# Optimization experiments

Measured on AMD Instinct MI355X. Metric: run time of the kernel, lower is better.

Reference implementation:

```python
import jax, jax.numpy as jnp
import numpy as np

B, L, D = 2, 2048, 2048
H, KV, HD = 16, 8, 128
EPS = 1e-5
ROPE_BASE = 10000.0
SCALING_ALPHA = 1.0
SCALE = HD ** -0.5


def setup_inputs() -> dict:
    key = jax.random.key(0)
    ks = jax.random.split(key, 5)
    s = 0.02  # weight init scale
    return {
        "x": jax.random.normal(ks[0], (B, L, D), jnp.float32),
        "wq": jax.random.normal(ks[1], (D, H * HD), jnp.float32) * s,
        "wk": jax.random.normal(ks[2], (D, KV * HD), jnp.float32) * s,
        "wv": jax.random.normal(ks[3], (D, KV * HD), jnp.float32) * s,
        "wo": jax.random.normal(ks[4], (H * HD, D), jnp.float32) * s,
        "qn_w": jnp.ones((HD,), jnp.float32),
        "kn_w": jnp.ones((HD,), jnp.float32),
    }


def _rope(t):
    # t: [B, h, L, HD]. DynamicNTKAlpha base scaling (alpha=1 -> no-op).
    base = ROPE_BASE * SCALING_ALPHA ** (HD / (HD - 2))
    # NOTE: source uses base**(+i/d) (no negative exponent) -- kept faithful.
    freqs = base ** (jnp.arange(0, HD, 2, dtype=jnp.float32) / HD)  # [HD/2]
    pos = jnp.arange(t.shape[-2], dtype=jnp.float32)                # [L]
    angles = pos[:, None] * freqs[None, :]                          # [L, HD/2]
    cos, sin = jnp.cos(angles), jnp.sin(angles)
    x1, x2 = t[..., : HD // 2], t[..., HD // 2 :]
    return jnp.concatenate([x1 * cos - x2 * sin, x2 * cos + x1 * sin], axis=-1)


def _rmsnorm(t, w):
    return t * jax.lax.rsqrt(jnp.mean(t * t, axis=-1, keepdims=True) + EPS) * w


def reference(x, wq, wk, wv, wo, qn_w, kn_w):
    b, l, _ = x.shape
    q = (x @ wq).reshape(b, l, H, HD).transpose(0, 2, 1, 3)   # [B,H,L,HD]
    k = (x @ wk).reshape(b, l, KV, HD).transpose(0, 2, 1, 3)  # [B,KV,L,HD]
    v = (x @ wv).reshape(b, l, KV, HD).transpose(0, 2, 1, 3)
    q = _rmsnorm(_rope(q), qn_w)
    k = _rmsnorm(_rope(k), kn_w)
    # GQA: expand KV heads to match query heads
    rep = H // KV
    k = jnp.repeat(k, rep, axis=1)  # [B,H,L,HD]
    v = jnp.repeat(v, rep, axis=1)
    scores = jnp.einsum("bhqd,bhkd->bhqk", q, k) * SCALE
    probs = jax.nn.softmax(scores, axis=-1)
    out = jnp.einsum("bhqk,bhkd->bhqd", probs, v)             # [B,H,L,HD]
    out = out.transpose(0, 2, 1, 3).reshape(b, l, H * HD)
    return out @ wo
```

## Files before the change

### kernel.cpp

```cpp
#include <hip/hip_runtime.h>
#include <math.h>

#define BB 2
#define LL 2048
#define DD 2048
#define HH 16
#define KVH 8
#define HDIM 128
#define SCALE_F 0.08838834764831845f
#define EPS_F 1e-5f
#define LOG2E 1.4426950408889634f
#define SMAX_F 17.0f
#define QKVW 4096

typedef unsigned short u16;
typedef __attribute__((ext_vector_type(8))) short short8;
typedef __attribute__((ext_vector_type(4))) float f32x4;
typedef __attribute__((ext_vector_type(16))) float f32x16;

#define MFMA16(a, b, c) __builtin_amdgcn_mfma_f32_16x16x32_bf16((a), (b), (c), 0, 0, 0)
#define MFMA32(a, b, c) __builtin_amdgcn_mfma_f32_32x32x16_bf16((a), (b), (c), 0, 0, 0)

__device__ __forceinline__ float b2f(u16 u) {
    union { unsigned int i; float f; } x;
    x.i = ((unsigned int)u) << 16;
    return x.f;
}
__device__ __forceinline__ u16 f2b(float f) {
    unsigned int x = __float_as_uint(f);
    unsigned int r = x + 0x7FFFu + ((x >> 16) & 1u);
    return (u16)(r >> 16);
}
__device__ __forceinline__ unsigned cvtpk(float lo, float hi) {
    unsigned r;
    asm("v_cvt_pk_bf16_f32 %0, %1, %2" : "=v"(r) : "v"(lo), "v"(hi));
    return r;
}
__device__ __forceinline__ void pl32swap(unsigned &a, unsigned &b) {
    asm("v_permlane32_swap_b32 %0, %1" : "+v"(a), "+v"(b));
}
__device__ __forceinline__ void g2l(const u16* g, u16* l) {
    __builtin_amdgcn_global_load_lds(
        (const __attribute__((address_space(1))) unsigned int*)g,
        (__attribute__((address_space(3))) unsigned int*)l, 16, 0, 0);
}

__global__ __launch_bounds__(256) void prep_kernel(const float* __restrict__ x,
                                                   u16* __restrict__ xb,
                                                   const float* __restrict__ wq,
                                                   const float* __restrict__ wk,
                                                   const float* __restrict__ wv,
                                                   const float* __restrict__ wo,
                                                   u16* __restrict__ wqkvT,
                                                   u16* __restrict__ woT,
                                                   float* __restrict__ ct,
                                                   float* __restrict__ st) {
    __shared__ u16 t[64 * 65];
    const int blk = blockIdx.x, tid = threadIdx.x;
    if (blk < 8192) {
        int i = (blk * 256 + tid) * 4;
        float4 v = *(const float4*)(x + i);
        unsigned int p0 = (unsigned int)f2b(v.x) | ((unsigned int)f2b(v.y) << 16);
        unsigned int p1 = (unsigned int)f2b(v.z) | ((unsigned int)f2b(v.w) << 16);
        uint2 pk; pk.x = p0; pk.y = p1;
        *(uint2*)(xb + i) = pk;
    } else if (blk < 11264) {
        int j = blk - 8192;
        const float* in; u16* out; int C, bx, by;
        if (j < 1024)      { in = wq; out = wqkvT;                      C = 2048; bx = j & 31; by = j >> 5; }
        else if (j < 1536) { j -= 1024; in = wk; out = wqkvT + (size_t)2048 * DD; C = 1024; bx = j & 15; by = j >> 4; }
        else if (j < 2048) { j -= 1536; in = wv; out = wqkvT + (size_t)3072 * DD; C = 1024; bx = j & 15; by = j >> 4; }
        else               { j -= 2048; in = wo; out = woT;                      C = 2048; bx = j & 31; by = j >> 5; }
        int c0 = bx * 64, r0 = by * 64;
#pragma unroll
        for (int i = 0; i < 16; i++) {
            int idx = tid + i * 256;
            int r = idx >> 6, c = idx & 63;
            t[r * 65 + c] = f2b(in[(size_t)(r0 + r) * C + c0 + c]);
        }
        __syncthreads();
#pragma unroll
        for (int i = 0; i < 16; i++) {
            int idx = tid + i * 256;
            int r = idx >> 6, c = idx & 63;
            out[(size_t)(c0 + r) * DD + r0 + c] = t[c * 65 + r];
        }
    } else {
        int i = (blk - 11264) * 256 + tid;
        int pos = i >> 6, d = i & 63;
        float freq = (float)pow(10000.0, (double)d * (1.0 / 64.0));
        float ang = (float)pos * freq;
        double a = (double)ang;
        ct[i] = (float)cos(a);
        st[i] = (float)sin(a);
    }
}

__global__ __launch_bounds__(256) void gemm_bt(const u16* __restrict__ A,
                                               const u16* __restrict__ Bt,
                                               u16* __restrict__ C, int M, int N, int K) {
    __shared__ __align__(16) u16 As[128 * 64];
    __shared__ __align__(16) u16 Bs[128 * 64];
    const int tid = threadIdx.x;
    const int w = tid >> 6, lane = tid & 63;
    const int lm = lane & 15, lq = lane >> 4;
    const int bn0 = blockIdx.x * 128, bm0 = blockIdx.y * 128;
    const int wm = (w >> 1) * 64, wn = (w & 1) * 64;

    f32x4 acc[4][4];
#pragma unroll
    for (int i = 0; i < 4; i++)
#pragma unroll
        for (int j = 0; j < 4; j++) acc[i][j] = (f32x4){0.f, 0.f, 0.f, 0.f};

    const int srow = lane >> 3;
    const int sgr = (lane & 7) ^ (srow & 7);
    const u16* ga = A + (size_t)(bm0 + w * 32 + srow) * K + sgr * 8;
    const u16* gb = Bt + (size_t)(bn0 + w * 32 + srow) * K + sgr * 8;
    u16* lA = &As[(w * 32) * 64];
    u16* lB = &Bs[(w * 32) * 64];

    for (int k0 = 0; k0 < K; k0 += 64) {
        __syncthreads();
#pragma unroll
        for (int ch = 0; ch < 4; ch++)
            g2l(ga + (size_t)(ch * 8) * K + k0, lA + ch * 8 * 64);
#pragma unroll
        for (int ch = 0; ch < 4; ch++)
            g2l(gb + (size_t)(ch * 8) * K + k0, lB + ch * 8 * 64);
        __syncthreads();

#pragma unroll
        for (int sub = 0; sub < 2; sub++) {
            short8 af[4], bf[4];
#pragma unroll
            for (int mt = 0; mt < 4; mt++) {
                int row = wm + mt * 16 + lm;
                af[mt] = *(const short8*)(&As[row * 64 + ((sub * 4 + lq) ^ (lm & 7)) * 8]);
            }
#pragma unroll
            for (int nt = 0; nt < 4; nt++) {
                int row = wn + nt * 16 + lm;
                bf[nt] = *(const short8*)(&Bs[row * 64 + ((sub * 4 + lq) ^ (lm & 7)) * 8]);
            }
#pragma unroll
            for (int mt = 0; mt < 4; mt++)
#pragma unroll
                for (int nt = 0; nt < 4; nt++) acc[mt][nt] = MFMA16(af[mt], bf[nt], acc[mt][nt]);
        }
    }

#pragma unroll
    for (int mt = 0; mt < 4; mt++)
#pragma unroll
        for (int nt = 0; nt < 4; nt++)
#pragma unroll
            for (int r = 0; r < 4; r++) {
                int row = bm0 + wm + mt * 16 + lq * 4 + r;
                int col = bn0 + wn + nt * 16 + lm;
                C[(size_t)row * N + col] = f2b(acc[mt][nt][r]);
            }
}

__global__ __launch_bounds__(256) void gemm_bt_o(const u16* __restrict__ A,
                                                 const u16* __restrict__ Bt,
                                                 float* __restrict__ C, int M, int N, int K) {
    __shared__ __align__(16) u16 As[64 * 64];
    __shared__ __align__(16) u16 Bs[128 * 64];
    const int tid = threadIdx.x;
    const int w = tid >> 6, lane = tid & 63;
    const int lm = lane & 15, lq = lane >> 4;
    const int bn0 = blockIdx.x * 128, bm0 = blockIdx.y * 64;
    const int wm = (w >> 1) * 32, wn = (w & 1) * 64;

    f32x4 acc[2][4];
#pragma unroll
    for (int i = 0; i < 2; i++)
#pragma unroll
        for (int j = 0; j < 4; j++) acc[i][j] = (f32x4){0.f, 0.f, 0.f, 0.f};

    const int srow = lane >> 3;
    const int sgr = (lane & 7) ^ (srow & 7);
    const u16* ga = A + (size_t)(bm0 + w * 16 + srow) * K + sgr * 8;
    const u16* gb = Bt + (size_t)(bn0 + w * 32 + srow) * K + sgr * 8;
    u16* lA = &As[(w * 16) * 64];
    u16* lB = &Bs[(w * 32) * 64];

    for (int k0 = 0; k0 < K; k0 += 64) {
        __syncthreads();
#pragma unroll
        for (int ch = 0; ch < 2; ch++)
            g2l(ga + (size_t)(ch * 8) * K + k0, lA + ch * 8 * 64);
#pragma unroll
        for (int ch = 0; ch < 4; ch++)
            g2l(gb + (size_t)(ch * 8) * K + k0, lB + ch * 8 * 64);
        __syncthreads();

#pragma unroll
        for (int sub = 0; sub < 2; sub++) {
            short8 af[2], bf[4];
#pragma unroll
            for (int mt = 0; mt < 2; mt++) {
                int row = wm + mt * 16 + lm;
                af[mt] = *(const short8*)(&As[row * 64 + ((sub * 4 + lq) ^ (lm & 7)) * 8]);
            }
#pragma unroll
            for (int nt = 0; nt < 4; nt++) {
                int row = wn + nt * 16 + lm;
                bf[nt] = *(const short8*)(&Bs[row * 64 + ((sub * 4 + lq) ^ (lm & 7)) * 8]);
            }
#pragma unroll
            for (int mt = 0; mt < 2; mt++)
#pragma unroll
                for (int nt = 0; nt < 4; nt++) acc[mt][nt] = MFMA16(af[mt], bf[nt], acc[mt][nt]);
        }
    }

#pragma unroll
    for (int mt = 0; mt < 2; mt++)
#pragma unroll
        for (int nt = 0; nt < 4; nt++)
#pragma unroll
            for (int r = 0; r < 4; r++) {
                int row = bm0 + wm + mt * 16 + lq * 4 + r;
                int col = bn0 + wn + nt * 16 + lm;
                C[(size_t)row * N + col] = acc[mt][nt][r];
            }
}

__global__ __launch_bounds__(256) void ropetv_kernel(u16* __restrict__ qkv,
                                                     u16* __restrict__ vt,
                                                     const float* __restrict__ qw,
                                                     const float* __restrict__ kw,
                                                     const float* __restrict__ ct,
                                                     const float* __restrict__ st) {
    __shared__ u16 t[64 * 65];
    const int blk = blockIdx.x, tid = threadIdx.x;
    if (blk < 24576) {
        int slot = blk * 4 + (tid >> 6);
        int lane = tid & 63;
        int hh = slot % (HH + KVH);
        int row = slot / (HH + KVH);
        int pos = row & (LL - 1);

        u16* base = qkv + (size_t)row * QKVW + hh * HDIM;
        const float* w = (hh < HH) ? qw : kw;

        float x1 = b2f(base[lane]), x2 = b2f(base[lane + 64]);
        float c = ct[pos * 64 + lane], s = st[pos * 64 + lane];
        float r1 = x1 * c - x2 * s;
        float r2 = x2 * c + x1 * s;
        float ss = r1 * r1 + r2 * r2;
#pragma unroll
        for (int m = 1; m < 64; m <<= 1) ss += __shfl_xor(ss, m, 64);
        float sc = 1.0f / sqrtf(ss * (1.0f / 128.0f) + EPS_F);
        base[lane] = f2b(r1 * sc * w[lane]);
        base[lane + 64] = f2b(r2 * sc * w[lane + 64]);
    } else {
        int j = blk - 24576;
        int bx = j & 31, by = (j >> 5) & 1, bg = j >> 6;
        int l0 = bx * 64, d0 = by * 64;
        int b = bg >> 3, g = bg & 7;
        const u16* src = qkv + (size_t)b * LL * QKVW + 3072 + g * HDIM;
        u16* dst = vt + (size_t)bg * HDIM * LL;
#pragma unroll
        for (int i = 0; i < 16; i++) {
            int idx = tid + i * 256;
            int r = idx >> 6, c = idx & 63;
            t[r * 65 + c] = src[(size_t)(l0 + r) * QKVW + d0 + c];
        }
        __syncthreads();
#pragma unroll
        for (int i = 0; i < 16; i++) {
            int idx = tid + i * 256;
            int r = idx >> 6, c = idx & 63;
            dst[(size_t)(d0 + r) * LL + l0 + c] = t[c * 65 + r];
        }
    }
}

__global__ __launch_bounds__(256, 3) void attn_kernel(const u16* __restrict__ qkv,
                                                      const u16* __restrict__ vt,
                                                      u16* __restrict__ ob) {
    __shared__ __align__(16) u16 SM[2 * 64 * 128 + 128 * 64];
    u16* Vt = SM + 2 * 64 * 128;

    const int tid = threadIdx.x, w = tid >> 6, lane = tid & 63;
    const int l31 = lane & 31, lh = lane >> 5;
    const int qh = w & 1, kh = w >> 1;
    const int q0 = blockIdx.x * 64;
    const int bh = blockIdx.y, b = bh >> 4, hd = bh & 15, g = hd >> 1;

    const u16* kbase = qkv + (size_t)b * LL * QKVW + 2048 + g * HDIM;
    const u16* vtbase = vt + (size_t)(b * KVH + g) * HDIM * LL;

    const int krl = lane >> 4, kgl = lane & 15;
    const int vrl = lane >> 3, vgl = lane & 7;

#define STAGEK(tt, bi) do {                                                  \
        _Pragma("unroll")                                                    \
        for (int ch = 0; ch < 4; ch++) {                                     \
            int r_ = w * 16 + ch * 4 + krl;                                  \
            int gc_ = kgl ^ (r_ & 15);                                       \
            g2l(kbase + (size_t)((tt) * 64 + r_) * QKVW + gc_ * 8,           \
                SM + (bi) * 8192 + (w * 16 + ch * 4) * 128);                 \
        }                                                                    \
    } while (0)
#define STAGEV(tt) do {                                                      \
        _Pragma("unroll")                                                    \
        for (int ch = 0; ch < 4; ch++) {                                     \
            int r_ = w * 32 + ch * 8 + vrl;                                  \
            int gc_ = vgl ^ (r_ & 7);                                        \
            g2l(vtbase + (size_t)r_ * LL + (tt) * 64 + gc_ * 8,              \
                Vt + (w * 32 + ch * 8) * 64);                                \
        }                                                                    \
    } while (0)

    const int qrow = q0 + qh * 32 + l31;
    short8 aq[8];
    {
        const u16* qp = qkv + (size_t)(b * LL + qrow) * QKVW + hd * HDIM + lh * 8;
#pragma unroll
        for (int kk = 0; kk < 8; kk++) aq[kk] = *(const short8*)(qp + kk * 16);
    }

    f32x16 o[4];
#pragma unroll
    for (int i = 0; i < 4; i++)
#pragma unroll
        for (int r = 0; r < 16; r++) o[i][r] = 0.f;
    float psum = 0.f;
    const float SC2 = SCALE_F * LOG2E;
    const f32x16 fz = {};

    STAGEK(0, 0);
    asm volatile("s_waitcnt vmcnt(0)" ::: "memory");
    __builtin_amdgcn_s_barrier();

    for (int t = 0; t < LL / 64; t++) {
        const int cur = t & 1;
        const u16* Kc = SM + cur * 8192;
        STAGEV(t);
        STAGEK((t + 1) & (LL / 64 - 1), cur ^ 1);

        const int key = kh * 32 + l31;
        f32x16 s;
        __builtin_amdgcn_s_setprio(1);
        {
            int gg = lh ^ (key & 15);
            short8 kf = *(const short8*)(&Kc[key * 128 + gg * 8]);
            s = MFMA32(kf, aq[0], fz);
        }
#pragma unroll
        for (int kk = 1; kk < 8; kk++) {
            int gg = (kk * 2 + lh) ^ (key & 15);
            short8 kf = *(const short8*)(&Kc[key * 128 + gg * 8]);
            s = MFMA32(kf, aq[kk], s);
        }
        __builtin_amdgcn_s_setprio(0);

        float p[16];
#pragma unroll
        for (int r = 0; r < 16; r++) {
            p[r] = __builtin_amdgcn_exp2f(fmaf(s[r], SC2, -SMAX_F));
            psum += p[r];
        }
        unsigned pw[2][4];
#pragma unroll
        for (int half = 0; half < 2; half++) {
            int qb = half * 8;
            unsigned c0 = cvtpk(p[qb + 0], p[qb + 1]);
            unsigned c1 = cvtpk(p[qb + 2], p[qb + 3]);
            unsigned c2 = cvtpk(p[qb + 4], p[qb + 5]);
            unsigned c3 = cvtpk(p[qb + 6], p[qb + 7]);
            pl32swap(c0, c2);
            pl32swap(c1, c3);
            pw[half][0] = c0; pw[half][1] = c1; pw[half][2] = c2; pw[half][3] = c3;
        }

        asm volatile("s_waitcnt vmcnt(4)" ::: "memory");
        __builtin_amdgcn_s_barrier();

        __builtin_amdgcn_s_setprio(1);
#pragma unroll
        for (int kcl = 0; kcl < 2; kcl++) {
            int kc = kh * 2 + kcl;
            union { unsigned u[4]; short8 s8; } pu;
#pragma unroll
            for (int i = 0; i < 4; i++) pu.u[i] = pw[kcl][i];
#pragma unroll
            for (int dn = 0; dn < 4; dn++) {
                int d = dn * 32 + l31;
                int gv = ((kc * 2 + lh) ^ (d & 7)) * 8;
                short8 bv = *(const short8*)(&Vt[d * 64 + gv]);
                o[dn] = MFMA32(pu.s8, bv, o[dn]);
            }
        }
        __builtin_amdgcn_s_setprio(0);

        asm volatile("s_waitcnt vmcnt(0)" ::: "memory");
        __builtin_amdgcn_s_barrier();
    }
#undef STAGEK
#undef STAGEV

    psum += __shfl_xor(psum, 32, 64);

    __syncthreads();
    float* xo = (float*)SM;
    float* xp = xo + 2 * 64 * 68;
    if (kh == 1) {
        float* dst = xo + (qh * 64 + lane) * 68;
#pragma unroll
        for (int dn = 0; dn < 4; dn++)
#pragma unroll
            for (int r = 0; r < 16; r += 4)
                *(f32x4*)(dst + dn * 16 + r) =
                    (f32x4){o[dn][r], o[dn][r + 1], o[dn][r + 2], o[dn][r + 3]};
        xp[qh * 64 + lane] = psum;
    }
    __syncthreads();
    if (kh == 0) {
        const float* src = xo + (qh * 64 + lane) * 68;
        float inv = 1.0f / (psum + xp[qh * 64 + lane]);
        float invr[16];
#pragma unroll
        for (int r = 0; r < 16; r++) {
            int row = (r & 3) + 8 * (r >> 2) + 4 * lh;
            invr[r] = __shfl(inv, row, 32);
        }
        u16* obase = ob + (size_t)(b * LL + q0 + qh * 32) * (HH * HDIM) + hd * HDIM;
#pragma unroll
        for (int dn = 0; dn < 4; dn++)
#pragma unroll
            for (int r = 0; r < 16; r++) {
                int row = (r & 3) + 8 * (r >> 2) + 4 * lh;
                float v = o[dn][r] + src[dn * 16 + r];
                obase[(size_t)row * (HH * HDIM) + dn * 32 + l31] = f2b(v * invr[r]);
            }
    }
}

extern "C" void kernel_launch(void* const* d_in, const int* in_sizes, int n_in,
                              void* d_out, int out_size, void* d_ws, size_t ws_size,
                              hipStream_t stream) {
    const float* x  = (const float*)d_in[0];
    const float* wq = (const float*)d_in[1];
    const float* wk = (const float*)d_in[2];
    const float* wv = (const float*)d_in[3];
    const float* wo = (const float*)d_in[4];
    const float* qn = (const float*)d_in[5];
    const float* kn = (const float*)d_in[6];

    u16* ws = (u16*)d_ws;
    const size_t SZ_X = (size_t)BB * LL * DD;
    u16* xb    = ws;
    u16* qkv   = xb + SZ_X;
    u16* wqkvT = qkv + (size_t)BB * LL * QKVW;
    u16* woT   = wqkvT + (size_t)QKVW * DD;
    float* ct  = (float*)(woT + (size_t)DD * DD);
    float* st  = ct + (size_t)LL * 64;
    u16* att = xb;
    u16* vt  = wqkvT;

    prep_kernel<<<dim3(11776), dim3(256), 0, stream>>>(x, xb, wq, wk, wv, wo,
                                                       wqkvT, woT, ct, st);
    gemm_bt<<<dim3(QKVW / 128, BB * LL / 128), dim3(256), 0, stream>>>(xb, wqkvT, qkv, BB * LL, QKVW, DD);
    ropetv_kernel<<<dim3(25600), dim3(256), 0, stream>>>(qkv, vt, qn, kn, ct, st);
    attn_kernel<<<dim3(LL / 64, BB * HH), dim3(256), 0, stream>>>(qkv, vt, att);
    gemm_bt_o<<<dim3(DD / 128, BB * LL / 64), dim3(256), 0, stream>>>(att, woT, (float*)d_out, BB * LL, DD, DD);
}
```

Measured before the change: 367.2 us.

## Enlarge attention blocks to 128 queries, double-buffer V, remap blocks per XCD

The attention kernel now runs 512 threads per block over 128 query rows, so each staged K/V tile serves twice as many queries. V is double-buffered alongside K, which removes the intra-iteration wait and barrier, leaving one __syncthreads per tile. Block indices are remapped so that consecutive blocks on the same XCD share a batch-head and reuse KV in cache. The cost is larger LDS use per block and fewer blocks in the grid, which may reduce occupancy.

After: 449.8 us. +22.5%, slower.

```diff
diff --git a/kernel.cpp b/kernel.cpp
--- a/kernel.cpp
+++ b/kernel.cpp
@@ -279,17 +279,22 @@
     }
 }
 
-__global__ __launch_bounds__(256, 3) void attn_kernel(const u16* __restrict__ qkv,
+__global__ __launch_bounds__(512, 4) void attn_kernel(const u16* __restrict__ qkv,
                                                       const u16* __restrict__ vt,
                                                       u16* __restrict__ ob) {
-    __shared__ __align__(16) u16 SM[2 * 64 * 128 + 128 * 64];
-    u16* Vt = SM + 2 * 64 * 128;
+    __shared__ __align__(16) u16 SM[34816];
+    u16* Kt0 = SM;
+    u16* Vt0 = SM + 2 * 64 * 128;
 
     const int tid = threadIdx.x, w = tid >> 6, lane = tid & 63;
     const int l31 = lane & 31, lh = lane >> 5;
-    const int qh = w & 1, kh = w >> 1;
-    const int q0 = blockIdx.x * 64;
-    const int bh = blockIdx.y, b = bh >> 4, hd = bh & 15, g = hd >> 1;
+    const int qh = w >> 1, kh = w & 1;
+
+    const int bid = blockIdx.y * 16 + blockIdx.x;
+    const int xcd = bid & 7, idx = bid >> 3;
+    const int bh = xcd * 4 + (idx >> 4);
+    const int q0 = (idx & 15) * 128;
+    const int b = bh >> 4, hd = bh & 15, g = hd >> 1;
 
     const u16* kbase = qkv + (size_t)b * LL * QKVW + 2048 + g * HDIM;
     const u16* vtbase = vt + (size_t)(b * KVH + g) * HDIM * LL;
@@ -297,22 +302,20 @@
     const int krl = lane >> 4, kgl = lane & 15;
     const int vrl = lane >> 3, vgl = lane & 7;
 
-#define STAGEK(tt, bi) do {                                                  \
+#define STAGE(tt, bi) do {                                                   \
         _Pragma("unroll")                                                    \
-        for (int ch = 0; ch < 4; ch++) {                                     \
-            int r_ = w * 16 + ch * 4 + krl;                                  \
+        for (int ch = 0; ch < 2; ch++) {                                     \
+            int r_ = w * 8 + ch * 4 + krl;                                   \
             int gc_ = kgl ^ (r_ & 15);                                       \
             g2l(kbase + (size_t)((tt) * 64 + r_) * QKVW + gc_ * 8,           \
-                SM + (bi) * 8192 + (w * 16 + ch * 4) * 128);                 \
+                Kt0 + (bi) * 8192 + (w * 8 + ch * 4) * 128);                 \
         }                                                                    \
-    } while (0)
-#define STAGEV(tt) do {                                                      \
         _Pragma("unroll")                                                    \
-        for (int ch = 0; ch < 4; ch++) {                                     \
-            int r_ = w * 32 + ch * 8 + vrl;                                  \
+        for (int ch = 0; ch < 2; ch++) {                                     \
+            int r_ = w * 16 + ch * 8 + vrl;                                  \
             int gc_ = vgl ^ (r_ & 7);                                        \
             g2l(vtbase + (size_t)r_ * LL + (tt) * 64 + gc_ * 8,              \
-                Vt + (w * 32 + ch * 8) * 64);                                \
+                Vt0 + (bi) * 8192 + (w * 16 + ch * 8) * 64);                 \
         }                                                                    \
     } while (0)
 
@@ -333,15 +336,14 @@
     const float SC2 = SCALE_F * LOG2E;
     const f32x16 fz = {};
 
-    STAGEK(0, 0);
-    asm volatile("s_waitcnt vmcnt(0)" ::: "memory");
-    __builtin_amdgcn_s_barrier();
+    STAGE(0, 0);
+    __syncthreads();
 
     for (int t = 0; t < LL / 64; t++) {
         const int cur = t & 1;
-        const u16* Kc = SM + cur * 8192;
-        STAGEV(t);
-        STAGEK((t + 1) & (LL / 64 - 1), cur ^ 1);
+        const u16* Kc = Kt0 + cur * 8192;
+        const u16* Vc = Vt0 + cur * 8192;
+        STAGE((t + 1) & (LL / 64 - 1), cur ^ 1);
 
         const int key = kh * 32 + l31;
         f32x16 s;
@@ -378,9 +380,6 @@
             pw[half][0] = c0; pw[half][1] = c1; pw[half][2] = c2; pw[half][3] = c3;
         }
 
-        asm volatile("s_waitcnt vmcnt(4)" ::: "memory");
-        __builtin_amdgcn_s_barrier();
-
         __builtin_amdgcn_s_setprio(1);
 #pragma unroll
         for (int kcl = 0; kcl < 2; kcl++) {
@@ -392,37 +391,36 @@
             for (int dn = 0; dn < 4; dn++) {
                 int d = dn * 32 + l31;
                 int gv = ((kc * 2 + lh) ^ (d & 7)) * 8;
-                short8 bv = *(const short8*)(&Vt[d * 64 + gv]);
+                short8 bv = *(const short8*)(&Vc[d * 64 + gv]);
                 o[dn] = MFMA32(pu.s8, bv, o[dn]);
             }
         }
         __builtin_amdgcn_s_setprio(0);
 
-        asm volatile("s_waitcnt vmcnt(0)" ::: "memory");
-        __builtin_amdgcn_s_barrier();
-    }
-#undef STAGEK
-#undef STAGEV
+        __syncthreads();
+    }
+#undef STAGE
 
     psum += __shfl_xor(psum, 32, 64);
 
     __syncthreads();
     float* xo = (float*)SM;
-    float* xp = xo + 2 * 64 * 68;
+    float* xp = xo + 4 * 32 * 130;
     if (kh == 1) {
-        float* dst = xo + (qh * 64 + lane) * 68;
+        float* dst = xo + qh * (32 * 130);
 #pragma unroll
         for (int dn = 0; dn < 4; dn++)
 #pragma unroll
-            for (int r = 0; r < 16; r += 4)
-                *(f32x4*)(dst + dn * 16 + r) =
-                    (f32x4){o[dn][r], o[dn][r + 1], o[dn][r + 2], o[dn][r + 3]};
-        xp[qh * 64 + lane] = psum;
+            for (int r = 0; r < 16; r++) {
+                int row = (r & 3) + 8 * (r >> 2) + 4 * lh;
+                dst[row * 130 + dn * 32 + l31] = o[dn][r];
+            }
+        xp[qh * 32 + l31] = psum;
     }
     __syncthreads();
     if (kh == 0) {
-        const float* src = xo + (qh * 64 + lane) * 68;
-        float inv = 1.0f / (psum + xp[qh * 64 + lane]);
+        const float* src = xo + qh * (32 * 130);
+        float inv = 1.0f / (psum + xp[qh * 32 + l31]);
         float invr[16];
 #pragma unroll
         for (int r = 0; r < 16; r++) {
@@ -435,7 +433,7 @@
 #pragma unroll
             for (int r = 0; r < 16; r++) {
                 int row = (r & 3) + 8 * (r >> 2) + 4 * lh;
-                float v = o[dn][r] + src[dn * 16 + r];
+                float v = o[dn][r] + src[row * 130 + dn * 32 + l31];
                 obase[(size_t)row * (HH * HDIM) + dn * 32 + l31] = f2b(v * invr[r]);
             }
     }
@@ -467,6 +465,6 @@
                                                        wqkvT, woT, ct, st);
     gemm_bt<<<dim3(QKVW / 128, BB * LL / 128), dim3(256), 0, stream>>>(xb, wqkvT, qkv, BB * LL, QKVW, DD);
     ropetv_kernel<<<dim3(25600), dim3(256), 0, stream>>>(qkv, vt, qn, kn, ct, st);
-    attn_kernel<<<dim3(LL / 64, BB * HH), dim3(256), 0, stream>>>(qkv, vt, att);
+    attn_kernel<<<dim3(LL / 128, BB * HH), dim3(512), 0, stream>>>(qkv, vt, att);
     gemm_bt_o<<<dim3(DD / 128, BB * LL / 64), dim3(256), 0, stream>>>(att, woT, (float*)d_out, BB * LL, DD, DD);
 }
```
